# Performance work log

Measured on AMD Instinct MI355X. Metric: run time of the kernel, lower is better.

## Reference

```python
import jax, jax.numpy as jnp
import numpy as np

MARGIN = 200.0
EPS = 1e-6  # torch F.pairwise_distance default eps (added to the difference)


def setup_inputs() -> dict:
    key = jax.random.key(0)
    k1, k2, k3 = jax.random.split(key, 3)
    B2, T, D = 128, 1024, 1024  # 2*batch_size, snippets, feature dim
    scores = jax.random.normal(k1, (B2, T), dtype=jnp.float32)
    feats = jax.random.normal(k2, (B2, T, D), dtype=jnp.float32)
    targets = jax.random.uniform(k3, (B2, T), dtype=jnp.float32)
    return {"scores": scores, "feats": feats, "targets": targets}


def _bce_with_logits(logits, targets):
    # mean over all elements of max(x,0) - x*t + log(1+exp(-|x|))
    return jnp.mean(jnp.maximum(logits, 0.0) - logits * targets
                    + jnp.log1p(jnp.exp(-jnp.abs(logits))))


def _contrastive(M):
    # M: [2b, T] feature magnitudes (L1 norms). Split into normal / abnormal.
    b = M.shape[0] // 2
    n_f, a_f = M[:b], M[b:]
    # pairwise euclidean distance d_ij = ||n_i - a_j + eps||_2   [b, b]
    diff = n_f[:, None, :] - a_f[None, :, :] + EPS
    dist = jnp.sqrt(jnp.sum(diff * diff, axis=-1))
    d = jnp.square(jnp.maximum(MARGIN - dist, 0.0))
    # strict '<' in the torch loop => first flat occurrence of the min
    flat_idx = jnp.argmin(d.reshape(-1))
    i_star = flat_idx // b
    j_star = flat_idx % b
    min_d = d.reshape(-1)[flat_idx]
    loss_con = 0.001 * min_d
    # loss_n: sum_{i != i*} ||n_i - n_{i*} + eps||^2 / b
    dn = n_f - n_f[i_star] + EPS
    sq_n = jnp.sum(dn * dn, axis=-1)          # [b]
    loss_n = (jnp.sum(sq_n) - sq_n[i_star]) / b
    da = a_f - a_f[j_star] + EPS
    sq_a = jnp.sum(da * da, axis=-1)
    loss_a = (jnp.sum(sq_a) - sq_a[j_star]) / b
    return loss_con + loss_n + loss_a


def reference(scores, feats, targets):
    loss_cls = _bce_with_logits(scores, targets)
    mags = jnp.sum(jnp.abs(feats), axis=2)    # torch.norm(p=1, dim=2) -> [2b, T]
    loss_con = _contrastive(mags)
    return loss_cls + 0.001 * loss_con
```

## Files before the change

kernel.cpp:

```cpp
#include <hip/hip_runtime.h>
#include <math.h>

typedef float f32x4 __attribute__((ext_vector_type(4)));

#define NB2   128
#define NT    1024
#define ND    1024
#define BHALF 64
#define NROWS (NB2 * NT)
#define MARGIN_F 200.0f
#define EPS_F    1e-6f

#define MAGS_BLOCKS (NROWS / 4)
#define BCE_BLOCKS  128


__device__ __forceinline__ float wave_reduce_sum(float s) {
#pragma unroll
    for (int off = 32; off > 0; off >>= 1)
        s += __shfl_xor(s, off, 64);
    return s;
}

__global__ void mags_bce_kernel(const float* __restrict__ feats,
                                const float* __restrict__ scores,
                                const float* __restrict__ targets,
                                float* __restrict__ mags,
                                float* __restrict__ bce_part) {
    const int wave = threadIdx.x >> 6;
    const int lane = threadIdx.x & 63;

    if (blockIdx.x < MAGS_BLOCKS) {
        const int row = blockIdx.x * 4 + wave;
        const float* src = feats + (size_t)row * ND;
        float s = 0.0f;
#pragma unroll
        for (int it = 0; it < 4; ++it) {
            f32x4 v = __builtin_nontemporal_load(
                reinterpret_cast<const f32x4*>(src + lane * 4 + it * 256));
            s += fabsf(v.x) + fabsf(v.y) + fabsf(v.z) + fabsf(v.w);
        }
        s = wave_reduce_sum(s);
        if (lane == 0) mags[row] = s;
        return;
    }

    const int b   = blockIdx.x - MAGS_BLOCKS;
    const int idx = b * 256 + threadIdx.x;
    f32x4 l4 = reinterpret_cast<const f32x4*>(scores)[idx];
    f32x4 t4 = reinterpret_cast<const f32x4*>(targets)[idx];
    float s = 0.0f;
#pragma unroll
    for (int c = 0; c < 4; ++c) {
        float l = l4[c], t = t4[c];
        s += fmaxf(l, 0.0f) - l * t + log1pf(expf(-fabsf(l)));
    }
    s = wave_reduce_sum(s);
    __shared__ float lds[4];
    if (lane == 0) lds[wave] = s;
    __syncthreads();
    if (threadIdx.x == 0)
        bce_part[b] = lds[0] + lds[1] + lds[2] + lds[3];
}

__global__ void dist_kernel(const float* __restrict__ mags,
                            float* __restrict__ dmat) {
    const int wave = threadIdx.x >> 6;
    const int lane = threadIdx.x & 63;
    const int pair = blockIdx.x * 4 + wave;
    const int i = pair >> 6;
    const int j = pair & 63;
    const float* nf = mags + (size_t)i * NT;
    const float* af = mags + (size_t)(BHALF + j) * NT;
    float s = 0.0f;
#pragma unroll
    for (int it = 0; it < 4; ++it) {
        f32x4 a = *reinterpret_cast<const f32x4*>(nf + lane * 4 + it * 256);
        f32x4 b = *reinterpret_cast<const f32x4*>(af + lane * 4 + it * 256);
#pragma unroll
        for (int c = 0; c < 4; ++c) {
            float dx = a[c] - b[c] + EPS_F;
            s += dx * dx;
        }
    }
    s = wave_reduce_sum(s);
    if (lane == 0) {
        float dist = sqrtf(s);
        float m = MARGIN_F - dist;
        dmat[pair] = (m > 0.0f) ? m * m : 0.0f;
    }
}

__global__ void __launch_bounds__(1024)
mega_kernel(const float* __restrict__ mags,
            const float* __restrict__ dmat,
            const float* __restrict__ bce_part,
            float* __restrict__ out) {
    __shared__ float sval[16];
    __shared__ int   sidx[16];
    __shared__ float bpart2[2];
    __shared__ float partials[16];
    __shared__ float s_mind;
    __shared__ int   s_istar, s_jstar;
    __shared__ float s_bce;

    const int t    = threadIdx.x;
    const int wave = t >> 6;
    const int lane = t & 63;

    float best = INFINITY;
    int   bidx = 0x7FFFFFFF;
#pragma unroll
    for (int k = t; k < 4096; k += 1024) {
        float v = dmat[k];
        if (v < best || (v == best && k < bidx)) { best = v; bidx = k; }
    }
#pragma unroll
    for (int off = 32; off > 0; off >>= 1) {
        float v2 = __shfl_xor(best, off, 64);
        int   i2 = __shfl_xor(bidx, off, 64);
        if (v2 < best || (v2 == best && i2 < bidx)) { best = v2; bidx = i2; }
    }
    if (lane == 0) { sval[wave] = best; sidx[wave] = bidx; }

    if (t < 128) {
        float s = wave_reduce_sum(bce_part[t]);
        if (lane == 0) bpart2[wave] = s;
    }
    __syncthreads();

    if (t == 0) {
        float bv = sval[0]; int bi = sidx[0];
        for (int w = 1; w < 16; ++w)
            if (sval[w] < bv || (sval[w] == bv && sidx[w] < bi)) { bv = sval[w]; bi = sidx[w]; }
        s_mind  = bv;
        s_istar = bi >> 6;
        s_jstar = bi & 63;
        s_bce   = bpart2[0] + bpart2[1];
    }
    __syncthreads();

    const int  istar = s_istar, jstar = s_jstar;
    const bool is_a  = (wave >= 8);
    const int  row0  = is_a ? (BHALF + (wave - 8) * 8) : (wave * 8);
    const int  ref   = is_a ? (BHALF + jstar) : istar;
    const float* r1  = mags + (size_t)ref * NT;

    float s = 0.0f;
#pragma unroll
    for (int r = 0; r < 8; ++r) {
        const int row = row0 + r;
        if (row == ref) continue;
        const float* r0 = mags + (size_t)row * NT;
#pragma unroll
        for (int it = 0; it < 4; ++it) {
            f32x4 a = *reinterpret_cast<const f32x4*>(r0 + lane * 4 + it * 256);
            f32x4 b = *reinterpret_cast<const f32x4*>(r1 + lane * 4 + it * 256);
#pragma unroll
            for (int c = 0; c < 4; ++c) {
                float dx = a[c] - b[c] + EPS_F;
                s += dx * dx;
            }
        }
    }
    s = wave_reduce_sum(s);
    if (lane == 0) partials[wave] = s;
    __syncthreads();

    if (t == 0) {
        float ln = 0.0f, la = 0.0f;
        for (int w = 0; w < 8; ++w)  ln += partials[w];
        for (int w = 8; w < 16; ++w) la += partials[w];
        float bce      = s_bce / (float)NROWS;
        float contrast = 0.001f * s_mind + ln / (float)BHALF + la / (float)BHALF;
        out[0] = bce + 0.001f * contrast;
    }
}

extern "C" void kernel_launch(void* const* d_in, const int* in_sizes, int n_in,
                              void* d_out, int out_size, void* d_ws, size_t ws_size,
                              hipStream_t stream) {
    const float* scores  = (const float*)d_in[0];
    const float* feats   = (const float*)d_in[1];
    const float* targets = (const float*)d_in[2];
    float* out      = (float*)d_out;
    float* ws       = (float*)d_ws;
    float* bce_part = ws + 64;
    float* dmat     = ws + 1024;
    float* mags     = ws + 8192;

    mags_bce_kernel<<<MAGS_BLOCKS + BCE_BLOCKS, 256, 0, stream>>>(
        feats, scores, targets, mags, bce_part);
    dist_kernel<<<4096 / 4, 256, 0, stream>>>(mags, dmat);
    mega_kernel<<<1, 1024, 0, stream>>>(mags, dmat, bce_part, out);
}
```

Baseline: 98.29 us.

## Use persistent-row mags waves and precompute intra-half sums for every candidate reference row

The magnitude pass now uses a fixed grid of 2048 blocks, each wave looping over 16 rows, and folds the BCE computation into the first 128 blocks. The intra-class squared-distance sums, which used to run in the single-block final kernel after the argmin, are now computed speculatively for all 128 possible reference rows in extra blocks of the pairs kernel. The final kernel then only looks up the chosen rows. This removes a serial 1-block tail at the cost of about 64x redundant but parallel intra-class work.

```diff
diff --git a/kernel.cpp b/kernel.cpp
--- a/kernel.cpp
+++ b/kernel.cpp
@@ -11,8 +11,10 @@
 #define MARGIN_F 200.0f
 #define EPS_F    1e-6f
 
-#define MAGS_BLOCKS (NROWS / 4)
-#define BCE_BLOCKS  128
+#define MAGS_BLOCKS   2048
+#define WAVES_TOTAL   (MAGS_BLOCKS*4)
+#define ROWS_PER_WAVE (NROWS / WAVES_TOTAL)
+#define BCE_BLOCKS    128
 
 
 __device__ __forceinline__ float wave_reduce_sum(float s) {
@@ -22,87 +24,123 @@
     return s;
 }
 
-__global__ void mags_bce_kernel(const float* __restrict__ feats,
-                                const float* __restrict__ scores,
-                                const float* __restrict__ targets,
-                                float* __restrict__ mags,
-                                float* __restrict__ bce_part) {
+__global__ void __launch_bounds__(256, 8)
+main_kernel(const float* __restrict__ feats,
+            const float* __restrict__ scores,
+            const float* __restrict__ targets,
+            float* __restrict__ mags,
+            float* __restrict__ bce_part) {
     const int wave = threadIdx.x >> 6;
     const int lane = threadIdx.x & 63;
 
-    if (blockIdx.x < MAGS_BLOCKS) {
-        const int row = blockIdx.x * 4 + wave;
-        const float* src = feats + (size_t)row * ND;
+    if (blockIdx.x < BCE_BLOCKS) {
+        const int idx = blockIdx.x * 256 + threadIdx.x;
+        f32x4 l4 = reinterpret_cast<const f32x4*>(scores)[idx];
+        f32x4 t4 = reinterpret_cast<const f32x4*>(targets)[idx];
+        float s = 0.0f;
+#pragma unroll
+        for (int c = 0; c < 4; ++c) {
+            float l = l4[c], t = t4[c];
+            s += fmaxf(l, 0.0f) - l * t + log1pf(expf(-fabsf(l)));
+        }
+        s = wave_reduce_sum(s);
+        __shared__ float lds[4];
+        if (lane == 0) lds[wave] = s;
+        __syncthreads();
+        if (threadIdx.x == 0)
+            bce_part[blockIdx.x] = lds[0] + lds[1] + lds[2] + lds[3];
+    }
+
+    const int gwave = blockIdx.x * 4 + wave;
+    const float* base = feats + (size_t)gwave * ROWS_PER_WAVE * ND + lane * 4;
+    float* mout = mags + (size_t)gwave * ROWS_PER_WAVE;
+
+#pragma unroll 2
+    for (int r = 0; r < ROWS_PER_WAVE; ++r) {
+        const float* src = base + (size_t)r * ND;
         float s = 0.0f;
 #pragma unroll
         for (int it = 0; it < 4; ++it) {
             f32x4 v = __builtin_nontemporal_load(
-                reinterpret_cast<const f32x4*>(src + lane * 4 + it * 256));
+                reinterpret_cast<const f32x4*>(src + it * 256));
             s += fabsf(v.x) + fabsf(v.y) + fabsf(v.z) + fabsf(v.w);
         }
         s = wave_reduce_sum(s);
-        if (lane == 0) mags[row] = s;
+        if (lane == 0) mout[r] = s;
+    }
+}
+
+__global__ void pairs_kernel(const float* __restrict__ mags,
+                             float* __restrict__ dmat,
+                             float* __restrict__ V) {
+    __shared__ float p[4];
+    const int wave = threadIdx.x >> 6;
+    const int lane = threadIdx.x & 63;
+
+    if (blockIdx.x < 1024) {
+        const int pair = blockIdx.x * 4 + wave;
+        const int i = pair >> 6;
+        const int j = pair & 63;
+        const float* nf = mags + (size_t)i * NT + lane * 4;
+        const float* af = mags + (size_t)(BHALF + j) * NT + lane * 4;
+        float s = 0.0f;
+#pragma unroll
+        for (int it = 0; it < 4; ++it) {
+            f32x4 a = *reinterpret_cast<const f32x4*>(nf + it * 256);
+            f32x4 b = *reinterpret_cast<const f32x4*>(af + it * 256);
+#pragma unroll
+            for (int c = 0; c < 4; ++c) {
+                float dx = a[c] - b[c] + EPS_F;
+                s += dx * dx;
+            }
+        }
+        s = wave_reduce_sum(s);
+        if (lane == 0) {
+            float dist = sqrtf(s);
+            float m = MARGIN_F - dist;
+            dmat[pair] = (m > 0.0f) ? m * m : 0.0f;
+        }
         return;
     }
 
-    const int b   = blockIdx.x - MAGS_BLOCKS;
-    const int idx = b * 256 + threadIdx.x;
-    f32x4 l4 = reinterpret_cast<const f32x4*>(scores)[idx];
-    f32x4 t4 = reinterpret_cast<const f32x4*>(targets)[idx];
+    const int b    = blockIdx.x - 1024;
+    const int half = b >> 6;
+    const int i    = b & 63;
+    const float* rowi = mags + (size_t)(half * BHALF + i) * NT + lane * 4;
+    f32x4 ri[4];
+#pragma unroll
+    for (int it = 0; it < 4; ++it)
+        ri[it] = *reinterpret_cast<const f32x4*>(rowi + it * 256);
+
     float s = 0.0f;
-#pragma unroll
-    for (int c = 0; c < 4; ++c) {
-        float l = l4[c], t = t4[c];
-        s += fmaxf(l, 0.0f) - l * t + log1pf(expf(-fabsf(l)));
+    for (int j = wave; j < BHALF; j += 4) {
+        if (j == i) continue;
+        const float* rowj = mags + (size_t)(half * BHALF + j) * NT + lane * 4;
+#pragma unroll
+        for (int it = 0; it < 4; ++it) {
+            f32x4 vj = *reinterpret_cast<const f32x4*>(rowj + it * 256);
+#pragma unroll
+            for (int c = 0; c < 4; ++c) {
+                float dx = vj[c] - ri[it][c] + EPS_F;
+                s += dx * dx;
+            }
+        }
     }
     s = wave_reduce_sum(s);
-    __shared__ float lds[4];
-    if (lane == 0) lds[wave] = s;
+    if (lane == 0) p[wave] = s;
     __syncthreads();
     if (threadIdx.x == 0)
-        bce_part[b] = lds[0] + lds[1] + lds[2] + lds[3];
-}
-
-__global__ void dist_kernel(const float* __restrict__ mags,
-                            float* __restrict__ dmat) {
-    const int wave = threadIdx.x >> 6;
-    const int lane = threadIdx.x & 63;
-    const int pair = blockIdx.x * 4 + wave;
-    const int i = pair >> 6;
-    const int j = pair & 63;
-    const float* nf = mags + (size_t)i * NT;
-    const float* af = mags + (size_t)(BHALF + j) * NT;
-    float s = 0.0f;
-#pragma unroll
-    for (int it = 0; it < 4; ++it) {
-        f32x4 a = *reinterpret_cast<const f32x4*>(nf + lane * 4 + it * 256);
-        f32x4 b = *reinterpret_cast<const f32x4*>(af + lane * 4 + it * 256);
-#pragma unroll
-        for (int c = 0; c < 4; ++c) {
-            float dx = a[c] - b[c] + EPS_F;
-            s += dx * dx;
-        }
-    }
-    s = wave_reduce_sum(s);
-    if (lane == 0) {
-        float dist = sqrtf(s);
-        float m = MARGIN_F - dist;
-        dmat[pair] = (m > 0.0f) ? m * m : 0.0f;
-    }
+        V[b] = p[0] + p[1] + p[2] + p[3];
 }
 
 __global__ void __launch_bounds__(1024)
-mega_kernel(const float* __restrict__ mags,
-            const float* __restrict__ dmat,
+mega_kernel(const float* __restrict__ dmat,
             const float* __restrict__ bce_part,
+            const float* __restrict__ V,
             float* __restrict__ out) {
     __shared__ float sval[16];
     __shared__ int   sidx[16];
     __shared__ float bpart2[2];
-    __shared__ float partials[16];
-    __shared__ float s_mind;
-    __shared__ int   s_istar, s_jstar;
-    __shared__ float s_bce;
 
     const int t    = threadIdx.x;
     const int wave = t >> 6;
@@ -133,46 +171,12 @@
         float bv = sval[0]; int bi = sidx[0];
         for (int w = 1; w < 16; ++w)
             if (sval[w] < bv || (sval[w] == bv && sidx[w] < bi)) { bv = sval[w]; bi = sidx[w]; }
-        s_mind  = bv;
-        s_istar = bi >> 6;
-        s_jstar = bi & 63;
-        s_bce   = bpart2[0] + bpart2[1];
-    }
-    __syncthreads();
-
-    const int  istar = s_istar, jstar = s_jstar;
-    const bool is_a  = (wave >= 8);
-    const int  row0  = is_a ? (BHALF + (wave - 8) * 8) : (wave * 8);
-    const int  ref   = is_a ? (BHALF + jstar) : istar;
-    const float* r1  = mags + (size_t)ref * NT;
-
-    float s = 0.0f;
-#pragma unroll
-    for (int r = 0; r < 8; ++r) {
-        const int row = row0 + r;
-        if (row == ref) continue;
-        const float* r0 = mags + (size_t)row * NT;
-#pragma unroll
-        for (int it = 0; it < 4; ++it) {
-            f32x4 a = *reinterpret_cast<const f32x4*>(r0 + lane * 4 + it * 256);
-            f32x4 b = *reinterpret_cast<const f32x4*>(r1 + lane * 4 + it * 256);
-#pragma unroll
-            for (int c = 0; c < 4; ++c) {
-                float dx = a[c] - b[c] + EPS_F;
-                s += dx * dx;
-            }
-        }
-    }
-    s = wave_reduce_sum(s);
-    if (lane == 0) partials[wave] = s;
-    __syncthreads();
-
-    if (t == 0) {
-        float ln = 0.0f, la = 0.0f;
-        for (int w = 0; w < 8; ++w)  ln += partials[w];
-        for (int w = 8; w < 16; ++w) la += partials[w];
-        float bce      = s_bce / (float)NROWS;
-        float contrast = 0.001f * s_mind + ln / (float)BHALF + la / (float)BHALF;
+        const int istar = bi >> 6;
+        const int jstar = bi & 63;
+        float bce      = (bpart2[0] + bpart2[1]) / (float)NROWS;
+        float loss_n   = V[istar] / (float)BHALF;
+        float loss_a   = V[BHALF + jstar] / (float)BHALF;
+        float contrast = 0.001f * bv + loss_n + loss_a;
         out[0] = bce + 0.001f * contrast;
     }
 }
@@ -186,11 +190,11 @@
     float* out      = (float*)d_out;
     float* ws       = (float*)d_ws;
     float* bce_part = ws + 64;
+    float* V        = ws + 192;
     float* dmat     = ws + 1024;
     float* mags     = ws + 8192;
 
-    mags_bce_kernel<<<MAGS_BLOCKS + BCE_BLOCKS, 256, 0, stream>>>(
-        feats, scores, targets, mags, bce_part);
-    dist_kernel<<<4096 / 4, 256, 0, stream>>>(mags, dmat);
-    mega_kernel<<<1, 1024, 0, stream>>>(mags, dmat, bce_part, out);
-}
+    main_kernel <<<MAGS_BLOCKS, 256, 0, stream>>>(feats, scores, targets, mags, bce_part);
+    pairs_kernel<<<1024 + 128, 256, 0, stream>>>(mags, dmat, V);
+    mega_kernel <<<1, 1024, 0, stream>>>(dmat, bce_part, V, out);
+}
```

Result: slower. 104.5 us (+6.3%).
